# Optimization experiments

Hardware: AMD Instinct MI355X
Metric: run time of the kernel (lower is better)

## Reference

```python
import jax, jax.numpy as jnp
import numpy as np

VAR_CXCY = 0.1   # variances[0]
VAR_WH = 0.2     # variances[1]
MIN_OVERLAP = 0.5
NEG_POS_RATIO = 3


def cxcy_to_xyxy(b):
    return jnp.concatenate([b[:, :2] - b[:, 2:] / 2, b[:, :2] + b[:, 2:] / 2], axis=-1)


def jaccard(a, b):
    # a: [O,4] xyxy, b: [P,4] xyxy -> [O,P]
    lt = jnp.maximum(a[:, None, :2], b[None, :, :2])
    rb = jnp.minimum(a[:, None, 2:], b[None, :, 2:])
    wh = jnp.clip(rb - lt, 0.0)
    inter = wh[..., 0] * wh[..., 1]
    area_a = (a[:, 2] - a[:, 0]) * (a[:, 3] - a[:, 1])
    area_b = (b[:, 2] - b[:, 0]) * (b[:, 3] - b[:, 1])
    return inter / (area_a[:, None] + area_b[None, :] - inter)


def xyxy_to_gcxgcy(boxes, priors):
    # boxes: [P,4] xyxy matched per-prior; priors: [P,4] cxcywh
    cxcy = (boxes[:, :2] + boxes[:, 2:]) / 2
    wh = boxes[:, 2:] - boxes[:, :2]
    g_cxcy = (cxcy - priors[:, :2]) / (priors[:, 2:] * VAR_CXCY)
    g_wh = jnp.log(wh / priors[:, 2:]) / VAR_WH
    return jnp.concatenate([g_cxcy, g_wh], axis=-1)


def _match_one(boxes, labels, priors, priors_xyxy):
    # boxes: [O,4] xyxy, labels: [O] int
    overlaps = jaccard(boxes, priors_xyxy)          # [O,P]
    prior_overlaps = overlaps.max(axis=0)            # [P]
    prior_objects = overlaps.argmax(axis=0)          # [P]
    object_priors = overlaps.argmax(axis=1)          # [O] best prior per object
    n_obj = boxes.shape[0]
    prior_objects = prior_objects.at[object_priors].set(jnp.arange(n_obj))
    prior_overlaps = prior_overlaps.at[object_priors].set(1.0)
    lab = labels[prior_objects]
    lab = jnp.where(prior_overlaps < MIN_OVERLAP, 0, lab)
    locs = xyxy_to_gcxgcy(boxes[prior_objects], priors)
    return locs, lab


def setup_inputs() -> dict:
    key = jax.random.key(0)
    B, P, C, O = 64, 8732, 81, 16
    ks = jax.random.split(key, 6)
    predict_locs = jax.random.normal(ks[0], (B, P, 4), dtype=jnp.float32)
    predict_confs = jax.random.normal(ks[1], (B, P, C), dtype=jnp.float32)
    # priors in cxcywh, valid sizes
    p_cxcy = jax.random.uniform(ks[2], (P, 2), minval=0.0, maxval=1.0)
    p_wh = jax.random.uniform(ks[2], (P, 2), minval=0.05, maxval=0.3)
    priors = jnp.concatenate([p_cxcy, p_wh], axis=-1).astype(jnp.float32)
    # targets: valid xyxy boxes in [0,1]
    t_cxcy = jax.random.uniform(ks[3], (B, O, 2), minval=0.2, maxval=0.8)
    t_wh = jax.random.uniform(ks[4], (B, O, 2), minval=0.05, maxval=0.4)
    target_boxes = jnp.concatenate([t_cxcy - t_wh / 2, t_cxcy + t_wh / 2], axis=-1).astype(jnp.float32)
    target_labels = jax.random.randint(ks[5], (B, O), 1, C)
    return {
        'predict_locs': predict_locs,
        'predict_confs': predict_confs,
        'target_boxes': target_boxes,
        'target_labels': target_labels,
        'priors': priors,
    }


def reference(predict_locs, predict_confs, target_boxes, target_labels, priors):
    priors_xyxy = cxcy_to_xyxy(priors)
    true_locs, true_confs = jax.vmap(
        lambda b, l: _match_one(b, l, priors, priors_xyxy)
    )(target_boxes, target_labels)              # [B,P,4], [B,P]

    pos = true_confs != 0                        # [B,P]
    n_pos = pos.sum(axis=1)                      # [B]
    n_pos_total = n_pos.sum().astype(predict_locs.dtype)

    # nn.L1Loss(reduction='mean') over the [n_pos_total, 4] gathered entries
    loc_loss = jnp.sum(jnp.abs(predict_locs - true_locs) * pos[..., None]) / (n_pos_total * 4)

    logp = jax.nn.log_softmax(predict_confs, axis=-1)
    ce = -jnp.take_along_axis(logp, true_confs[..., None], axis=-1)[..., 0]  # [B,P]

    ce_pos_sum = jnp.sum(jnp.where(pos, ce, 0.0))
    ce_neg = jnp.where(pos, 0.0, ce)
    # double-sort rank: rank of each prior when sorted by descending neg loss
    rank = jnp.argsort(jnp.argsort(-ce_neg, axis=1), axis=1)
    hard = rank < (NEG_POS_RATIO * n_pos)[:, None]
    ce_hard_sum = jnp.sum(jnp.where(hard, ce_neg, 0.0))

    conf_loss = (ce_hard_sum + ce_pos_sum) / n_pos_total
    return conf_loss + loc_loss
```

## Files before the change

kernel.cpp:

```cpp
#include <hip/hip_runtime.h>
#include <cstdint>
#include <cstddef>

constexpr int O_C   = 16;
constexpr int P_MAX = 8732;
constexpr int CH    = 4;
constexpr int CHP   = 2183;

__device__ __forceinline__ float waveSumF(float v) {
    #pragma unroll
    for (int off = 32; off; off >>= 1) v += __shfl_xor(v, off);
    return v;
}
__device__ __forceinline__ int waveSumI(int v) {
    #pragma unroll
    for (int off = 32; off; off >>= 1) v += __shfl_xor(v, off);
    return v;
}

__global__ __launch_bounds__(256) void lse_match(
    const float* __restrict__ confs,
    const float* __restrict__ target_boxes,
    const float* __restrict__ priors,
    float* __restrict__ ov_out,
    unsigned char* __restrict__ obj_out,
    unsigned long long* __restrict__ okey_part,
    float* __restrict__ lse_out,
    int P, int nlse)
{
    const int tid  = threadIdx.x;
    const int lane = tid & 63;
    const int wid  = tid >> 6;

    __shared__ float s_x[64 * 81 + 4];
    __shared__ float bx0[O_C], by0[O_C], bx1[O_C], by1[O_C], barea[O_C];
    __shared__ unsigned long long s_wb[O_C * 4];

    if (blockIdx.x < (unsigned)nlse) {
        const size_t tbase = (size_t)blockIdx.x * 64 * 81;
        {
            const float4* src = reinterpret_cast<const float4*>(confs + tbase);
            float4* dst = reinterpret_cast<float4*>(s_x);
            #pragma unroll
            for (int k = 0; k < 6; ++k) {
                int i = tid + k * 256;
                if (i < 1296) dst[i] = src[i];
            }
        }
        __syncthreads();

        const int rl = tid >> 2;
        const int q  = tid & 3;
        const int s0 = q ? (q * 20 + 1) : 0;
        const int n  = q ? 20 : 21;
        const float* xr = s_x + rl * 81;

        float v[21];
        #pragma unroll
        for (int i = 0; i < 21; ++i)
            v[i] = (i < n) ? xr[s0 + i] : -3.0e38f;

        float m = v[0];
        #pragma unroll
        for (int i = 1; i < 21; ++i) m = fmaxf(m, v[i]);
        m = fmaxf(m, __shfl_xor(m, 1));
        m = fmaxf(m, __shfl_xor(m, 2));

        float s = 0.0f;
        #pragma unroll
        for (int i = 0; i < 21; ++i)
            if (i < n) s += __expf(v[i] - m);
        s += __shfl_xor(s, 1);
        s += __shfl_xor(s, 2);

        if (q == 0)
            lse_out[(size_t)blockIdx.x * 64 + rl] = m + __logf(s);
        return;
    }

    const int chunk = blockIdx.x - nlse;
    const int b = chunk / CH;
    const int c = chunk % CH;

    if (tid < O_C) {
        const float* tb = target_boxes + ((size_t)b * O_C + tid) * 4;
        float x0 = tb[0], y0 = tb[1], x1 = tb[2], y1 = tb[3];
        bx0[tid] = x0; by0[tid] = y0; bx1[tid] = x1; by1[tid] = y1;
        barea[tid] = (x1 - x0) * (y1 - y0);
    }
    __syncthreads();

    float bi[O_C]; int bp[O_C];
    #pragma unroll
    for (int o = 0; o < O_C; ++o) { bi[o] = -1.0f; bp[o] = 0; }

    const int p0 = c * CHP, p1 = min(p0 + CHP, P);
    for (int p = p0 + tid; p < p1; p += 256) {
        float4 pr = reinterpret_cast<const float4*>(priors)[p];
        float px0 = pr.x - pr.z * 0.5f, py0 = pr.y - pr.w * 0.5f;
        float px1 = pr.x + pr.z * 0.5f, py1 = pr.y + pr.w * 0.5f;
        float parea = (px1 - px0) * (py1 - py0);
        float bv = -1.0f; int bo = 0;
        #pragma unroll
        for (int o = 0; o < O_C; ++o) {
            float ix0 = fmaxf(px0, bx0[o]), iy0 = fmaxf(py0, by0[o]);
            float ix1 = fminf(px1, bx1[o]), iy1 = fminf(py1, by1[o]);
            float iw = fmaxf(ix1 - ix0, 0.0f), ih = fmaxf(iy1 - iy0, 0.0f);
            float inter = iw * ih;
            float iou = inter / (barea[o] + parea - inter);
            if (iou > bv) { bv = iou; bo = o; }
            if (iou > bi[o]) { bi[o] = iou; bp[o] = p; }
        }
        ov_out[(size_t)b * P + p]  = bv;
        obj_out[(size_t)b * P + p] = (unsigned char)bo;
    }

    #pragma unroll
    for (int o = 0; o < O_C; ++o) {
        unsigned long long k = (bi[o] >= 0.0f)
            ? (((unsigned long long)__float_as_uint(bi[o]) << 32) |
               (unsigned long long)(0xFFFFFFFFu - (unsigned)bp[o]))
            : 0ull;
        #pragma unroll
        for (int off = 32; off; off >>= 1) {
            unsigned long long k2 = __shfl_xor(k, off);
            if (k2 > k) k = k2;
        }
        if (lane == 0) s_wb[o * 4 + wid] = k;
    }
    __syncthreads();
    if (tid < O_C) {
        unsigned long long k = s_wb[tid * 4];
        #pragma unroll
        for (int w = 1; w < 4; ++w) if (s_wb[tid * 4 + w] > k) k = s_wb[tid * 4 + w];
        okey_part[(size_t)chunk * O_C + tid] = k;
    }
}

__global__ __launch_bounds__(1024) void hard_kernel(
    const float* __restrict__ confs,
    const float* __restrict__ lse,
    const float* __restrict__ ov_in,
    const unsigned char* __restrict__ obj_in,
    const unsigned long long* __restrict__ okey_part,
    const float* __restrict__ target_boxes,
    const int*   __restrict__ target_labels,
    const float* __restrict__ priors,
    const float* __restrict__ predict_locs,
    int*   __restrict__ n_pos,
    float* __restrict__ ce_pos,
    float* __restrict__ ce_hard,
    float* __restrict__ loc_b,
    int P)
{
    const int b    = blockIdx.x;
    const int tid  = threadIdx.x;
    const int lane = tid & 63;
    const int wid  = tid >> 6;

    __shared__ float s_v[P_MAX];
    __shared__ unsigned int hist[16][256];
    __shared__ float4 tbox[O_C];
    __shared__ int    tlab[O_C], topr[O_C];
    __shared__ unsigned int s_sel;
    __shared__ int s_kr;
    __shared__ float s_f[16], s_f2[16], s_f3[16];
    __shared__ int s_i[16];

    if (tid < O_C) {
        const float* tb = target_boxes + ((size_t)b * O_C + tid) * 4;
        tbox[tid] = make_float4(tb[0], tb[1], tb[2], tb[3]);
        tlab[tid] = target_labels[(size_t)b * O_C + tid];
        unsigned long long kk = 0ull;
        #pragma unroll
        for (int cc = 0; cc < CH; ++cc) {
            unsigned long long k2 = okey_part[((size_t)b * CH + cc) * O_C + tid];
            if (k2 > kk) kk = k2;
        }
        topr[tid] = (int)(0xFFFFFFFFu - (unsigned)(kk & 0xFFFFFFFFull));
    }
    __syncthreads();

    const size_t base = (size_t)b * P;
    float possum = 0.0f, negsum = 0.0f, locsum = 0.0f;
    int cnt = 0;
    for (int p = tid; p < P; p += 1024) {
        float ovv = ov_in[base + p];
        int   obj = obj_in[base + p];
        #pragma unroll
        for (int o = 0; o < O_C; ++o)
            if (topr[o] == p) { obj = o; ovv = 1.0f; }
        const int l = (ovv < 0.5f) ? 0 : tlab[obj];
        float xl  = confs[(base + p) * 81 + l];
        float cev = lse[base + p] - xl;
        if (l != 0) {
            possum += cev; ++cnt;
            s_v[p] = 0.0f;
            float4 pr = reinterpret_cast<const float4*>(priors)[p];
            float4 tb = tbox[obj];
            float cx = (tb.x + tb.z) * 0.5f, cy = (tb.y + tb.w) * 0.5f;
            float w  = tb.z - tb.x,          h  = tb.w - tb.y;
            float g0 = (cx - pr.x) / (pr.z * 0.1f);
            float g1 = (cy - pr.y) / (pr.w * 0.1f);
            float g2 = logf(w / pr.z) / 0.2f;
            float g3 = logf(h / pr.w) / 0.2f;
            float4 pl = reinterpret_cast<const float4*>(predict_locs)[base + p];
            locsum += fabsf(pl.x - g0) + fabsf(pl.y - g1) +
                      fabsf(pl.z - g2) + fabsf(pl.w - g3);
        } else {
            negsum += cev;
            s_v[p] = cev;
        }
    }
    possum = waveSumF(possum);
    negsum = waveSumF(negsum);
    locsum = waveSumF(locsum);
    cnt    = waveSumI(cnt);
    if (lane == 0) { s_f[wid] = possum; s_f2[wid] = negsum; s_f3[wid] = locsum; s_i[wid] = cnt; }
    __syncthreads();
    float negsum_t = 0.0f, possum_t = 0.0f, locsum_t = 0.0f; int np = 0;
    #pragma unroll
    for (int w = 0; w < 16; ++w) {
        negsum_t += s_f2[w]; possum_t += s_f[w]; locsum_t += s_f3[w]; np += s_i[w];
    }
    if (tid == 0) { ce_pos[b] = possum_t; n_pos[b] = np; loc_b[b] = locsum_t; }

    const int K = 3 * np;
    if (K <= 0) { if (tid == 0) ce_hard[b] = 0.0f; return; }
    if (K >= P) { if (tid == 0) ce_hard[b] = negsum_t; return; }

    unsigned int prefix = 0; int kr = K;
    for (int shift = 24; shift >= 0; shift -= 8) {
        for (int i = tid; i < 16 * 256; i += 1024) (&hist[0][0])[i] = 0;
        __syncthreads();
        unsigned int maskHi = (shift == 24) ? 0u : (0xFFFFFFFFu << (shift + 8));
        for (int p = tid; p < P; p += 1024) {
            unsigned int u = __float_as_uint(s_v[p]);
            if ((u & maskHi) == prefix) atomicAdd(&hist[wid][(u >> shift) & 255], 1u);
        }
        __syncthreads();
        if (wid == 0) {
            unsigned h0 = 0, h1 = 0, h2 = 0, h3 = 0;
            #pragma unroll 4
            for (int w = 0; w < 16; ++w) {
                h0 += hist[w][lane * 4 + 0];
                h1 += hist[w][lane * 4 + 1];
                h2 += hist[w][lane * 4 + 2];
                h3 += hist[w][lane * 4 + 3];
            }
            unsigned own = h0 + h1 + h2 + h3;
            unsigned t = own;
            #pragma unroll
            for (int off = 1; off < 64; off <<= 1) {
                unsigned u = __shfl_down(t, off);
                if (lane + off >= 64) u = 0;
                t += u;
            }
            unsigned Tnext = t - own;
            unsigned cum3 = Tnext;
            unsigned cum2 = cum3 + h3;
            unsigned cum1 = cum2 + h2;
            unsigned cum0 = cum1 + h1;
            unsigned kru = (unsigned)kr;
            int selj = -1; unsigned cg = 0;
            if      (cum3 < kru && kru <= cum3 + h3) { selj = 3; cg = cum3; }
            else if (cum2 < kru && kru <= cum2 + h2) { selj = 2; cg = cum2; }
            else if (cum1 < kru && kru <= cum1 + h1) { selj = 1; cg = cum1; }
            else if (cum0 < kru && kru <= cum0 + h0) { selj = 0; cg = cum0; }
            if (selj >= 0) {
                s_sel = prefix | ((unsigned)(lane * 4 + selj) << shift);
                s_kr  = kr - (int)cg;
            }
        }
        __syncthreads();
        prefix = s_sel; kr = s_kr;
        __syncthreads();
    }

    float sumgt = 0.0f;
    for (int p = tid; p < P; p += 1024) {
        unsigned int u = __float_as_uint(s_v[p]);
        if (u > prefix) sumgt += s_v[p];
    }
    sumgt = waveSumF(sumgt);
    if (lane == 0) s_f[wid] = sumgt;
    __syncthreads();
    if (tid == 0) {
        float sg = 0.0f;
        #pragma unroll
        for (int w = 0; w < 16; ++w) sg += s_f[w];
        ce_hard[b] = sg + (float)kr * __uint_as_float(prefix);
    }
}

__global__ __launch_bounds__(64) void finalize_kernel(
    const int*   __restrict__ n_pos,
    const float* __restrict__ ce_pos,
    const float* __restrict__ ce_hard,
    const float* __restrict__ loc_b,
    float* __restrict__ out, int B)
{
    const int lane = threadIdx.x;
    int np = 0; float cp = 0.0f, ch = 0.0f, la = 0.0f;
    for (int b = lane; b < B; b += 64) {
        np += n_pos[b]; cp += ce_pos[b]; ch += ce_hard[b]; la += loc_b[b];
    }
    #pragma unroll
    for (int off = 32; off; off >>= 1) {
        np += __shfl_xor(np, off);
        cp += __shfl_xor(cp, off);
        ch += __shfl_xor(ch, off);
        la += __shfl_xor(la, off);
    }
    if (lane == 0) {
        float npt = (float)np;
        out[0] = (ch + cp) / npt + la / (npt * 4.0f);
    }
}

extern "C" void kernel_launch(void* const* d_in, const int* in_sizes, int n_in,
                              void* d_out, int out_size, void* d_ws, size_t ws_size,
                              hipStream_t stream) {
    const float* predict_locs  = (const float*)d_in[0];
    const float* predict_confs = (const float*)d_in[1];
    const float* target_boxes  = (const float*)d_in[2];
    const int*   target_labels = (const int*)d_in[3];
    const float* priors        = (const float*)d_in[4];

    const int P = in_sizes[4] / 4;
    const int B = in_sizes[0] / (P * 4);
    const int rows = B * P;
    const int nmatch = B * CH;
    const int nlse = rows / 64;

    char* ws = (char*)d_ws;
    unsigned long long* okey_part = (unsigned long long*)ws;
    ws += (size_t)nmatch * O_C * sizeof(unsigned long long);
    float* lse     = (float*)ws; ws += (size_t)rows * sizeof(float);
    float* ov      = (float*)ws; ws += (size_t)rows * sizeof(float);
    int*   n_pos   = (int*)ws;   ws += (size_t)B * sizeof(int);
    float* ce_pos  = (float*)ws; ws += (size_t)B * sizeof(float);
    float* ce_hard = (float*)ws; ws += (size_t)B * sizeof(float);
    float* loc_b   = (float*)ws; ws += (size_t)B * sizeof(float);
    unsigned char* obj = (unsigned char*)ws; ws += (size_t)rows;

    lse_match<<<nlse + nmatch, 256, 0, stream>>>(
        predict_confs, target_boxes, priors, ov, obj, okey_part, lse, P, nlse);
    hard_kernel<<<B, 1024, 0, stream>>>(
        predict_confs, lse, ov, obj, okey_part, target_boxes, target_labels,
        priors, predict_locs, n_pos, ce_pos, ce_hard, loc_b, P);
    finalize_kernel<<<1, 64, 0, stream>>>(n_pos, ce_pos, ce_hard, loc_b,
                                          (float*)d_out, B);
}
```

Measured before the change: 94.72 us.

## Persist LSE blocks with async double-buffered LDS loads, recompute IoU in hard kernel

The log-sum-exp part becomes a persistent grid of 2048 blocks. Each block walks 64-row tiles and double-buffers them into LDS using global_load_lds async copies, so the next tile's load overlaps the current tile's compute. Matching blocks now produce only the per-object best-prior keys. The per-prior best overlap and object index are recomputed in hard_kernel instead of being written to and read back from global memory, trading extra IoU arithmetic for less memory traffic. Matching blocks are placed first in the grid so they start early.

```diff
diff --git a/kernel.cpp b/kernel.cpp
--- a/kernel.cpp
+++ b/kernel.cpp
@@ -6,6 +6,7 @@
 constexpr int P_MAX = 8732;
 constexpr int CH    = 4;
 constexpr int CHP   = 2183;
+constexpr int NCE   = 2048;
 
 __device__ __forceinline__ float waveSumF(float v) {
     #pragma unroll
@@ -18,43 +19,115 @@
     return v;
 }
 
+__device__ __forceinline__ void async_g2l16(const float* g, float* l) {
+    __builtin_amdgcn_global_load_lds(
+        (const __attribute__((address_space(1))) void*)g,
+        (__attribute__((address_space(3))) void*)l,
+        16, 0, 0);
+}
+
 __global__ __launch_bounds__(256) void lse_match(
     const float* __restrict__ confs,
     const float* __restrict__ target_boxes,
     const float* __restrict__ priors,
-    float* __restrict__ ov_out,
-    unsigned char* __restrict__ obj_out,
     unsigned long long* __restrict__ okey_part,
     float* __restrict__ lse_out,
-    int P, int nlse)
+    int P, int ntile, int nmatch)
 {
     const int tid  = threadIdx.x;
     const int lane = tid & 63;
     const int wid  = tid >> 6;
 
-    __shared__ float s_x[64 * 81 + 4];
+    __shared__ __align__(16) float s_t[2][5188];
     __shared__ float bx0[O_C], by0[O_C], bx1[O_C], by1[O_C], barea[O_C];
     __shared__ unsigned long long s_wb[O_C * 4];
 
-    if (blockIdx.x < (unsigned)nlse) {
-        const size_t tbase = (size_t)blockIdx.x * 64 * 81;
-        {
-            const float4* src = reinterpret_cast<const float4*>(confs + tbase);
-            float4* dst = reinterpret_cast<float4*>(s_x);
+    if (blockIdx.x < (unsigned)nmatch) {
+        const int chunk = blockIdx.x;
+        const int b = chunk / CH;
+        const int c = chunk % CH;
+
+        if (tid < O_C) {
+            const float* tb = target_boxes + ((size_t)b * O_C + tid) * 4;
+            float x0 = tb[0], y0 = tb[1], x1 = tb[2], y1 = tb[3];
+            bx0[tid] = x0; by0[tid] = y0; bx1[tid] = x1; by1[tid] = y1;
+            barea[tid] = (x1 - x0) * (y1 - y0);
+        }
+        __syncthreads();
+
+        float bi[O_C]; int bp[O_C];
+        #pragma unroll
+        for (int o = 0; o < O_C; ++o) { bi[o] = -1.0f; bp[o] = 0; }
+
+        const int p0 = c * CHP, p1 = min(p0 + CHP, P);
+        for (int p = p0 + tid; p < p1; p += 256) {
+            float4 pr = reinterpret_cast<const float4*>(priors)[p];
+            float px0 = pr.x - pr.z * 0.5f, py0 = pr.y - pr.w * 0.5f;
+            float px1 = pr.x + pr.z * 0.5f, py1 = pr.y + pr.w * 0.5f;
+            float parea = (px1 - px0) * (py1 - py0);
             #pragma unroll
-            for (int k = 0; k < 6; ++k) {
-                int i = tid + k * 256;
-                if (i < 1296) dst[i] = src[i];
-            }
-        }
-        __syncthreads();
-
-        const int rl = tid >> 2;
-        const int q  = tid & 3;
-        const int s0 = q ? (q * 20 + 1) : 0;
-        const int n  = q ? 20 : 21;
-        const float* xr = s_x + rl * 81;
-
+            for (int o = 0; o < O_C; ++o) {
+                float ix0 = fmaxf(px0, bx0[o]), iy0 = fmaxf(py0, by0[o]);
+                float ix1 = fminf(px1, bx1[o]), iy1 = fminf(py1, by1[o]);
+                float iw = fmaxf(ix1 - ix0, 0.0f), ih = fmaxf(iy1 - iy0, 0.0f);
+                float inter = iw * ih;
+                float iou = inter / (barea[o] + parea - inter);
+                if (iou > bi[o]) { bi[o] = iou; bp[o] = p; }
+            }
+        }
+
+        #pragma unroll
+        for (int o = 0; o < O_C; ++o) {
+            unsigned long long k = (bi[o] >= 0.0f)
+                ? (((unsigned long long)__float_as_uint(bi[o]) << 32) |
+                   (unsigned long long)(0xFFFFFFFFu - (unsigned)bp[o]))
+                : 0ull;
+            #pragma unroll
+            for (int off = 32; off; off >>= 1) {
+                unsigned long long k2 = __shfl_xor(k, off);
+                if (k2 > k) k = k2;
+            }
+            if (lane == 0) s_wb[o * 4 + wid] = k;
+        }
+        __syncthreads();
+        if (tid < O_C) {
+            unsigned long long k = s_wb[tid * 4];
+            #pragma unroll
+            for (int w = 1; w < 4; ++w) if (s_wb[tid * 4 + w] > k) k = s_wb[tid * 4 + w];
+            okey_part[(size_t)chunk * O_C + tid] = k;
+        }
+        return;
+    }
+
+    const int bt0 = blockIdx.x - nmatch;
+    const int rl = tid >> 2;
+    const int q  = tid & 3;
+    const int s0 = q ? (q * 20 + 1) : 0;
+    const int n  = q ? 20 : 21;
+
+    auto stage = [&](int buf, int t) {
+        const float* src = confs + (size_t)t * 5184;
+        #pragma unroll
+        for (int c = 0; c < 5; ++c) {
+            async_g2l16(src + (size_t)(c * 256 + tid) * 4,
+                        &s_t[buf][(c * 256 + wid * 64) * 4]);
+        }
+        if (tid < 16) {
+            float4 v = reinterpret_cast<const float4*>(src)[1280 + tid];
+            reinterpret_cast<float4*>(&s_t[buf][5120])[tid] = v;
+        }
+    };
+
+    if (bt0 >= ntile) return;
+    stage(0, bt0);
+    __syncthreads();
+
+    for (int t = bt0, k = 0; t < ntile; t += NCE, ++k) {
+        const int cur = k & 1;
+        const int tn = t + NCE;
+        if (tn < ntile) stage(cur ^ 1, tn);
+
+        const float* xr = &s_t[cur][rl * 81];
         float v[21];
         #pragma unroll
         for (int i = 0; i < 21; ++i)
@@ -74,74 +147,15 @@
         s += __shfl_xor(s, 2);
 
         if (q == 0)
-            lse_out[(size_t)blockIdx.x * 64 + rl] = m + __logf(s);
-        return;
-    }
-
-    const int chunk = blockIdx.x - nlse;
-    const int b = chunk / CH;
-    const int c = chunk % CH;
-
-    if (tid < O_C) {
-        const float* tb = target_boxes + ((size_t)b * O_C + tid) * 4;
-        float x0 = tb[0], y0 = tb[1], x1 = tb[2], y1 = tb[3];
-        bx0[tid] = x0; by0[tid] = y0; bx1[tid] = x1; by1[tid] = y1;
-        barea[tid] = (x1 - x0) * (y1 - y0);
-    }
-    __syncthreads();
-
-    float bi[O_C]; int bp[O_C];
-    #pragma unroll
-    for (int o = 0; o < O_C; ++o) { bi[o] = -1.0f; bp[o] = 0; }
-
-    const int p0 = c * CHP, p1 = min(p0 + CHP, P);
-    for (int p = p0 + tid; p < p1; p += 256) {
-        float4 pr = reinterpret_cast<const float4*>(priors)[p];
-        float px0 = pr.x - pr.z * 0.5f, py0 = pr.y - pr.w * 0.5f;
-        float px1 = pr.x + pr.z * 0.5f, py1 = pr.y + pr.w * 0.5f;
-        float parea = (px1 - px0) * (py1 - py0);
-        float bv = -1.0f; int bo = 0;
-        #pragma unroll
-        for (int o = 0; o < O_C; ++o) {
-            float ix0 = fmaxf(px0, bx0[o]), iy0 = fmaxf(py0, by0[o]);
-            float ix1 = fminf(px1, bx1[o]), iy1 = fminf(py1, by1[o]);
-            float iw = fmaxf(ix1 - ix0, 0.0f), ih = fmaxf(iy1 - iy0, 0.0f);
-            float inter = iw * ih;
-            float iou = inter / (barea[o] + parea - inter);
-            if (iou > bv) { bv = iou; bo = o; }
-            if (iou > bi[o]) { bi[o] = iou; bp[o] = p; }
-        }
-        ov_out[(size_t)b * P + p]  = bv;
-        obj_out[(size_t)b * P + p] = (unsigned char)bo;
-    }
-
-    #pragma unroll
-    for (int o = 0; o < O_C; ++o) {
-        unsigned long long k = (bi[o] >= 0.0f)
-            ? (((unsigned long long)__float_as_uint(bi[o]) << 32) |
-               (unsigned long long)(0xFFFFFFFFu - (unsigned)bp[o]))
-            : 0ull;
-        #pragma unroll
-        for (int off = 32; off; off >>= 1) {
-            unsigned long long k2 = __shfl_xor(k, off);
-            if (k2 > k) k = k2;
-        }
-        if (lane == 0) s_wb[o * 4 + wid] = k;
-    }
-    __syncthreads();
-    if (tid < O_C) {
-        unsigned long long k = s_wb[tid * 4];
-        #pragma unroll
-        for (int w = 1; w < 4; ++w) if (s_wb[tid * 4 + w] > k) k = s_wb[tid * 4 + w];
-        okey_part[(size_t)chunk * O_C + tid] = k;
+            lse_out[(size_t)t * 64 + rl] = m + __logf(s);
+
+        __syncthreads();
     }
 }
 
 __global__ __launch_bounds__(1024) void hard_kernel(
     const float* __restrict__ confs,
     const float* __restrict__ lse,
-    const float* __restrict__ ov_in,
-    const unsigned char* __restrict__ obj_in,
     const unsigned long long* __restrict__ okey_part,
     const float* __restrict__ target_boxes,
     const int*   __restrict__ target_labels,
@@ -161,6 +175,7 @@
     __shared__ float s_v[P_MAX];
     __shared__ unsigned int hist[16][256];
     __shared__ float4 tbox[O_C];
+    __shared__ float  tarea[O_C];
     __shared__ int    tlab[O_C], topr[O_C];
     __shared__ unsigned int s_sel;
     __shared__ int s_kr;
@@ -169,8 +184,10 @@
 
     if (tid < O_C) {
         const float* tb = target_boxes + ((size_t)b * O_C + tid) * 4;
-        tbox[tid] = make_float4(tb[0], tb[1], tb[2], tb[3]);
-        tlab[tid] = target_labels[(size_t)b * O_C + tid];
+        float x0 = tb[0], y0 = tb[1], x1 = tb[2], y1 = tb[3];
+        tbox[tid]  = make_float4(x0, y0, x1, y1);
+        tarea[tid] = (x1 - x0) * (y1 - y0);
+        tlab[tid]  = target_labels[(size_t)b * O_C + tid];
         unsigned long long kk = 0ull;
         #pragma unroll
         for (int cc = 0; cc < CH; ++cc) {
@@ -185,18 +202,33 @@
     float possum = 0.0f, negsum = 0.0f, locsum = 0.0f;
     int cnt = 0;
     for (int p = tid; p < P; p += 1024) {
-        float ovv = ov_in[base + p];
-        int   obj = obj_in[base + p];
+        float4 pr = reinterpret_cast<const float4*>(priors)[p];
+        float px0 = pr.x - pr.z * 0.5f, py0 = pr.y - pr.w * 0.5f;
+        float px1 = pr.x + pr.z * 0.5f, py1 = pr.y + pr.w * 0.5f;
+        float parea = (px1 - px0) * (py1 - py0);
+        float bv = -1.0f; int bo = 0;
+        #pragma unroll
+        for (int o = 0; o < O_C; ++o) {
+            float4 tb = tbox[o];
+            float ix0 = fmaxf(px0, tb.x), iy0 = fmaxf(py0, tb.y);
+            float ix1 = fminf(px1, tb.z), iy1 = fminf(py1, tb.w);
+            float iw = fmaxf(ix1 - ix0, 0.0f), ih = fmaxf(iy1 - iy0, 0.0f);
+            float inter = iw * ih;
+            float iou = inter / (tarea[o] + parea - inter);
+            if (iou > bv) { bv = iou; bo = o; }
+        }
+        float ovv = bv;
+        int   obj = bo;
         #pragma unroll
         for (int o = 0; o < O_C; ++o)
             if (topr[o] == p) { obj = o; ovv = 1.0f; }
         const int l = (ovv < 0.5f) ? 0 : tlab[obj];
+
         float xl  = confs[(base + p) * 81 + l];
         float cev = lse[base + p] - xl;
         if (l != 0) {
             possum += cev; ++cnt;
             s_v[p] = 0.0f;
-            float4 pr = reinterpret_cast<const float4*>(priors)[p];
             float4 tb = tbox[obj];
             float cx = (tb.x + tb.z) * 0.5f, cy = (tb.y + tb.w) * 0.5f;
             float w  = tb.z - tb.x,          h  = tb.w - tb.y;
@@ -330,24 +362,22 @@
     const int P = in_sizes[4] / 4;
     const int B = in_sizes[0] / (P * 4);
     const int rows = B * P;
+    const int ntile = rows / 64;
     const int nmatch = B * CH;
-    const int nlse = rows / 64;
 
     char* ws = (char*)d_ws;
     unsigned long long* okey_part = (unsigned long long*)ws;
     ws += (size_t)nmatch * O_C * sizeof(unsigned long long);
     float* lse     = (float*)ws; ws += (size_t)rows * sizeof(float);
-    float* ov      = (float*)ws; ws += (size_t)rows * sizeof(float);
     int*   n_pos   = (int*)ws;   ws += (size_t)B * sizeof(int);
     float* ce_pos  = (float*)ws; ws += (size_t)B * sizeof(float);
     float* ce_hard = (float*)ws; ws += (size_t)B * sizeof(float);
     float* loc_b   = (float*)ws; ws += (size_t)B * sizeof(float);
-    unsigned char* obj = (unsigned char*)ws; ws += (size_t)rows;
-
-    lse_match<<<nlse + nmatch, 256, 0, stream>>>(
-        predict_confs, target_boxes, priors, ov, obj, okey_part, lse, P, nlse);
+
+    lse_match<<<nmatch + NCE, 256, 0, stream>>>(
+        predict_confs, target_boxes, priors, okey_part, lse, P, ntile, nmatch);
     hard_kernel<<<B, 1024, 0, stream>>>(
-        predict_confs, lse, ov, obj, okey_part, target_boxes, target_labels,
+        predict_confs, lse, okey_part, target_boxes, target_labels,
         priors, predict_locs, n_pos, ce_pos, ce_hard, loc_b, P);
     finalize_kernel<<<1, 64, 0, stream>>>(n_pos, ce_pos, ce_hard, loc_b,
                                           (float*)d_out, B);
```

Result: slower. 108.3 us (+14.4%).
